# Kernel optimization log

Hardware: AMD Instinct MI355X
Metric: run time of the kernel (lower is better)

Reference implementation:

```python
import jax, jax.numpy as jnp
import numpy as np

B, N, D, K, C = 8, 4096, 128, 16, 64  # batch, points, in_channels, knn, growth_rate


def _knn_idx(pos, k):
    # pos: (B, N, 3); returns (B, N, k) nearest-neighbor indices excluding self (offset=1)
    sq = jnp.sum(pos * pos, axis=-1)  # (B, N)
    d2 = sq[:, :, None] + sq[:, None, :] - 2.0 * jnp.einsum('bnd,bmd->bnm', pos, pos)
    _, idx = jax.lax.top_k(-d2, k + 1)  # sorted ascending by distance
    return idx[:, :, 1:]


def _knn_group(x, idx):
    # x: (B, N, F), idx: (B, N, K) -> (B, N, K, F)
    return jax.vmap(lambda xb, ib: xb[ib])(x, idx)


def setup_inputs():
    key = jax.random.key(0)
    ks = jax.random.split(key, 10)
    sc = 0.05
    return {
        'x': jax.random.normal(ks[0], (B, N, D), jnp.float32),
        'pos': jax.random.normal(ks[1], (B, N, 3), jnp.float32),
        'W_first': jax.random.normal(ks[2], (3 * D, C), jnp.float32) * sc,
        'b_first': jnp.zeros((C,), jnp.float32),
        'W_mid1': jax.random.normal(ks[3], (D + C, C), jnp.float32) * sc,
        'b_mid1': jnp.zeros((C,), jnp.float32),
        'W_mid2': jax.random.normal(ks[4], (D + 2 * C, C), jnp.float32) * sc,
        'b_mid2': jnp.zeros((C,), jnp.float32),
        'W_last': jax.random.normal(ks[5], (D + 3 * C, C), jnp.float32) * sc,
        'b_last': jnp.zeros((C,), jnp.float32),
    }


def reference(x, pos, W_first, b_first, W_mid1, b_mid1, W_mid2, b_mid2, W_last, b_last):
    knn_idx = _knn_idx(pos, K)                      # (B, N, K)
    knn_feat = _knn_group(x, knn_idx)               # (B, N, K, D)
    x_tiled = jnp.broadcast_to(x[:, :, None, :], knn_feat.shape)
    edge_feat = jnp.concatenate([x_tiled, knn_feat, knn_feat - x_tiled], axis=-1)  # (B,N,K,3D)

    y = jnp.concatenate([jax.nn.relu(edge_feat @ W_first + b_first), x_tiled], axis=-1)  # (B,N,K,D+C)
    y = jnp.concatenate([jax.nn.relu(y @ W_mid1 + b_mid1), y], axis=-1)                  # (B,N,K,D+2C)
    y = jnp.concatenate([jax.nn.relu(y @ W_mid2 + b_mid2), y], axis=-1)                  # (B,N,K,D+3C)
    y = jnp.concatenate([y @ W_last + b_last, y], axis=-1)                               # (B,N,K,D+4C)
    return jnp.max(y, axis=2)                       # (B, N, D+4C)
```

## Files before the change

kernel.cpp:

```cpp
#include <hip/hip_runtime.h>
#include <hip/hip_bf16.h>

typedef unsigned int uint;
typedef unsigned short ushort_t;
typedef unsigned long long u64;
typedef __attribute__((ext_vector_type(8))) short short8;
typedef __attribute__((ext_vector_type(4))) float floatx4;

#define NB 8
#define NP 4096
#define ND 128
#define NK 16
#define NC 64
#define NPTS 32768
#define QB 16
#define CAP4 208
#define NQE 8

__device__ __forceinline__ float bf2f(ushort_t h){ return __uint_as_float(((uint)h)<<16); }
__device__ __forceinline__ ushort_t f2bf(float f){
  uint u = __float_as_uint(f);
  u = u + 0x7FFFu + ((u>>16)&1u);
  return (ushort_t)(u>>16);
}
__device__ __forceinline__ float ldin(const void* p, long i, int f32){
  return f32 ? ((const float*)p)[i] : bf2f(((const ushort_t*)p)[i]);
}
__device__ __forceinline__ void stout(void* o, long i, float v, int f32){
  if (f32) ((float*)o)[i] = v; else ((ushort_t*)o)[i] = f2bf(v);
}

#define SWZE(row, e) (((row)<<6) + ((e) ^ (((row)&7)<<3)))
#define WAVE_SYNC() asm volatile("s_waitcnt lgkmcnt(0)" ::: "memory")

__global__ __launch_bounds__(256) void k_detect(const uint* __restrict__ w, int* __restrict__ flag){
  __shared__ int cnt;
  if (threadIdx.x == 0) cnt = 0;
  __syncthreads();
  int c = 0;
  for (int i = threadIdx.x; i < 512; i += 256){
    uint u = w[i];
    uint e = (u >> 7) & 0xFFu;
    c += (e >= 100u && e < 128u) ? 1 : 0;
  }
  atomicAdd(&cnt, c);
  __syncthreads();
  if (threadIdx.x == 0) *flag = (cnt < 256) ? 1 : 0;
}

__global__ __launch_bounds__(256) void k_posf(const void* __restrict__ pos, float4* __restrict__ posf,
                                              const int* __restrict__ flag){
#pragma clang fp contract(off)
  int f32 = *flag;
  int p = blockIdx.x*256 + threadIdx.x;
  if (p >= NPTS) return;
  float x = ldin(pos, (long)p*3+0, f32);
  float y = ldin(pos, (long)p*3+1, f32);
  float z = ldin(pos, (long)p*3+2, f32);
  float px = x*x; float py = y*y; float pz = z*z;
  float sq = (px + py) + pz;
  posf[p] = make_float4(x, y, z, sq);
}

__global__ __launch_bounds__(256) void k_knn(const float4* __restrict__ posf, int* __restrict__ knn){
#pragma clang fp contract(off)
  __shared__ u64 scand[QB][CAP4];
  __shared__ int scnt[QB];
  __shared__ uint sut[QB];
  int tid = threadIdx.x;
  int lane = tid & 63;
  int wave = tid >> 6;
  int qbase = blockIdx.x * QB;
  int jbase = (qbase >> 12) << 12;
  if (tid < QB){ scnt[tid] = 0; sut[tid] = 0xFFFFFFFFu; }
  __syncthreads();
  float4 Q[QB];
  #pragma unroll
  for (int q = 0; q < QB; ++q) Q[q] = posf[qbase + q];
  float lmf[QB];
  #pragma unroll
  for (int q = 0; q < QB; ++q) lmf[q] = 3.0e38f;
  for (int s = 0; s < 16; ++s){
    float4 p = posf[jbase + s*256 + tid];
    #pragma unroll
    for (int q = 0; q < QB; ++q){
      float dot = __builtin_fmaf(Q[q].x, p.x, __builtin_fmaf(Q[q].y, p.y, Q[q].z * p.z));
      float v   = __builtin_fmaf(-2.0f, dot, Q[q].w + p.w);
      lmf[q] = fminf(lmf[q], v);
    }
  }
  uint lmb[QB];
  #pragma unroll
  for (int q = 0; q < QB; ++q) lmb[q] = __float_as_uint(fmaxf(lmf[q], 0.0f));
  #pragma unroll
  for (int q = 0; q < QB; ++q){
    int lo = 0, hi = 4095;
    while (lo < hi){
      int mid = (lo + hi) >> 1;
      uint T = (uint)(mid+1) << 19;
      u64 bal = __ballot(lmb[q] < T);
      if (__popcll(bal) >= 17) hi = mid; else lo = mid + 1;
    }
    if (lane == 0) atomicMin(&sut[q], (uint)(lo+2) << 19);
  }
  __syncthreads();
  uint utq[QB];
  #pragma unroll
  for (int q = 0; q < QB; ++q) utq[q] = sut[q];
  for (int s = 0; s < 16; ++s){
    int j = s*256 + tid;
    float4 p = posf[jbase + j];
    #pragma unroll
    for (int q = 0; q < QB; ++q){
      float ax = Q[q].x*p.x; float ay = Q[q].y*p.y; float az = Q[q].z*p.z;
      float dot = (ax + ay) + az;
      float t  = Q[q].w + p.w;
      float v  = t - 2.0f*dot;
      uint ubv = __float_as_uint(fmaxf(v, 0.0f));
      if (ubv < utq[q]){
        int pc = atomicAdd(&scnt[q], 1);
        if (pc < CAP4){
          uint w = __float_as_uint(v);
          uint sd = w ^ ((w & 0x80000000u) ? 0xFFFFFFFFu : 0x80000000u);
          scand[q][pc] = (((u64)sd) << 32) | (uint)j;
        }
      }
    }
  }
  __syncthreads();
  for (int q = wave; q < QB; q += 4){
    int cnt = scnt[q]; if (cnt > CAP4) cnt = CAP4;
    for (int base = 0; base < cnt; base += 64){
      int ci = base + lane;
      u64 mykey = (ci < cnt) ? scand[q][ci] : ~0ull;
      int r = 0;
      for (int i = 0; i < cnt; ++i) r += (scand[q][i] < mykey) ? 1 : 0;
      if (ci < cnt && r >= 1 && r <= 16)
        knn[(qbase + q)*16 + (r-1)] = (int)(mykey & 0xFFFFFFFFu);
    }
  }
}

__global__ __launch_bounds__(256) void k_wprep(const void* __restrict__ Wf, const void* __restrict__ bfv,
                        const void* __restrict__ Wm1, const void* __restrict__ bm1,
                        const void* __restrict__ Wm2, const void* __restrict__ bm2,
                        const void* __restrict__ Wl, const void* __restrict__ bl,
                        ushort_t* __restrict__ WcatT, float* __restrict__ biasT,
                        ushort_t* __restrict__ Wtiles,
                        const int* __restrict__ flag){
  int f32 = *flag;
  int id = blockIdx.x*256 + threadIdx.x;
  if (id < 40960){
    int n = id >> 7, k = id & 127;
    float v;
    if (n < 64)       v = ldin(Wf, (long)k*64 + n, f32) - ldin(Wf, (long)(256+k)*64 + n, f32);
    else if (n < 128) v = ldin(Wf, (long)(128+k)*64 + (n-64), f32) + ldin(Wf, (long)(256+k)*64 + (n-64), f32);
    else if (n < 192) v = ldin(Wm1, (long)(64+k)*64 + (n-128), f32);
    else if (n < 256) v = ldin(Wm2, (long)(128+k)*64 + (n-192), f32);
    else              v = ldin(Wl, (long)(192+k)*64 + (n-256), f32);
    WcatT[id] = f2bf(v);
  } else if (id < 41280){
    int n = id - 40960;
    float bv;
    if (n < 64)       bv = ldin(bfv, n, f32);
    else if (n < 128) bv = 0.0f;
    else if (n < 192) bv = ldin(bm1, n-128, f32);
    else if (n < 256) bv = ldin(bm2, n-192, f32);
    else              bv = ldin(bl, n-256, f32);
    biasT[n] = bv;
  } else if (id < 65856){
    int t2 = id - 41280;
    int tile = t2 >> 10;
    int r    = (t2 >> 6) & 15;
    int ep   = t2 & 63;
    int kl   = ep ^ ((r & 7) << 3);
    float v;
    if (tile < 4){
      int n = tile*16 + r;
      v = ldin(Wm1, (long)kl*64 + n, f32);
    } else if (tile < 12){
      int u = tile - 4; int n = (u >> 1)*16 + r; int k = (u & 1)*64 + kl;
      v = ldin(Wm2, (long)k*64 + n, f32);
    } else {
      int u = tile - 12; int n = (u / 3)*16 + r; int k = (u % 3)*64 + kl;
      v = ldin(Wl, (long)k*64 + n, f32);
    }
    Wtiles[t2] = f2bf(v);
  }
}

__global__ __launch_bounds__(256) void k_pgemm(const void* __restrict__ xv, const ushort_t* __restrict__ WcatT,
                                               const float* __restrict__ biasT, ushort_t* __restrict__ P,
                                               const int* __restrict__ flag){
  int f32 = *flag;
  int wave = threadIdx.x >> 6, lane = threadIdx.x & 63;
  int rowbase = blockIdx.x*64 + wave*16;
  int quad = lane >> 4, col = lane & 15;
  floatx4 acc[20];
  #pragma unroll
  for (int i = 0; i < 20; ++i) acc[i] = (floatx4){0.f,0.f,0.f,0.f};
  #pragma unroll
  for (int kk = 0; kk < 4; ++kk){
    int k = kk*32 + quad*8;
    short8 a;
    if (f32){
      const float* xf = (const float*)xv + (long)(rowbase + col)*128 + k;
      #pragma unroll
      for (int i = 0; i < 8; ++i) a[i] = (short)f2bf(xf[i]);
    } else {
      a = *(const short8*)((const ushort_t*)xv + (long)(rowbase + col)*128 + k);
    }
    #pragma unroll
    for (int nt = 0; nt < 20; ++nt){
      short8 bb = *(const short8*)(WcatT + (nt*16 + col)*128 + k);
      acc[nt] = __builtin_amdgcn_mfma_f32_16x16x32_bf16(a, bb, acc[nt], 0, 0, 0);
    }
  }
  #pragma unroll
  for (int nt = 0; nt < 20; ++nt){
    float bv = biasT[nt*16 + col];
    #pragma unroll
    for (int r = 0; r < 4; ++r){
      int m = quad*4 + r;
      P[(long)(rowbase + m)*320 + nt*16 + col] = f2bf(acc[nt][r] + bv);
    }
  }
}

__global__ __launch_bounds__(256) void k_edge(const void* __restrict__ x, const ushort_t* __restrict__ P,
                                              const int* __restrict__ knn,
                                              const ushort_t* __restrict__ Wg, void* __restrict__ out,
                                              const int* __restrict__ flag){
  __shared__ __align__(16) ushort_t wlds[24*1024];
  __shared__ __align__(16) ushort_t hb[4][3][1024];
  int f32 = *flag;
  int tid = threadIdx.x;
  int wave = tid >> 6, lane = tid & 63;
  int quad = lane >> 4, col = lane & 15;
  #pragma unroll
  for (int i = 0; i < 12; ++i){
    int e = (i*256 + tid) << 3;
    *(short8*)(wlds + e) = *(const short8*)(Wg + e);
  }
  __syncthreads();
  const ushort_t* wA = wlds;
  const ushort_t* wB = wlds + 4*1024;
  const ushort_t* wC = wlds + 12*1024;
  ushort_t* h1p = hb[wave][0];
  ushort_t* h2p = hb[wave][1];
  ushort_t* h3p = hb[wave][2];
  int qid0 = blockIdx.x*(4*NQE) + wave*NQE;

  for (int iq = 0; iq < NQE; ++iq){
    int qid = qid0 + iq;
    int b = qid >> 12;
    const ushort_t* Prow = P + (long)qid*320;
    long outb = (long)qid*384;

    float u1v[4], u2v[4], u3v[4];
    #pragma unroll
    for (int nt = 0; nt < 4; ++nt){
      u1v[nt] = bf2f(Prow[128 + nt*16 + col]);
      u2v[nt] = bf2f(Prow[192 + nt*16 + col]);
      u3v[nt] = bf2f(Prow[256 + nt*16 + col]);
    }

    {
      int e = lane >> 2, cg = lane & 3;
      int nbr = knn[qid*16 + e] & (NP - 1);
      const ushort_t* Pk = P + ((long)(b<<12) + nbr)*320 + 64 + cg*16;
      const ushort_t* Pq = Prow + cg*16;
      short8 k0 = *(const short8*)(Pk);
      short8 k1 = *(const short8*)(Pk + 8);
      short8 q0 = *(const short8*)(Pq);
      short8 q1 = *(const short8*)(Pq + 8);
      short8 h0, h1r;
      #pragma unroll
      for (int i = 0; i < 8; ++i){
        float v = fmaxf(bf2f((ushort_t)q0[i]) + bf2f((ushort_t)k0[i]), 0.0f);
        h0[i] = (short)f2bf(v);
        float w = fmaxf(bf2f((ushort_t)q1[i]) + bf2f((ushort_t)k1[i]), 0.0f);
        h1r[i] = (short)f2bf(w);
      }
      *(short8*)(h1p + SWZE(e, cg*16))     = h0;
      *(short8*)(h1p + SWZE(e, cg*16 + 8)) = h1r;
    }
    WAVE_SYNC();

    floatx4 acc2[4];
    #pragma unroll
    for (int nt = 0; nt < 4; ++nt) acc2[nt] = (floatx4){0.f,0.f,0.f,0.f};
    #pragma unroll
    for (int kk = 0; kk < 2; ++kk){
      int k = kk*32 + quad*8;
      short8 a = *(const short8*)(h1p + SWZE(col, k));
      #pragma unroll
      for (int nt = 0; nt < 4; ++nt){
        short8 bb = *(const short8*)(wA + nt*1024 + SWZE(col, k));
        acc2[nt] = __builtin_amdgcn_mfma_f32_16x16x32_bf16(a, bb, acc2[nt], 0, 0, 0);
      }
    }
    #pragma unroll
    for (int nt = 0; nt < 4; ++nt){
      float v0 = fmaxf(acc2[nt][0] + u1v[nt], 0.0f);
      float v1 = fmaxf(acc2[nt][1] + u1v[nt], 0.0f);
      float v2 = fmaxf(acc2[nt][2] + u1v[nt], 0.0f);
      float v3 = fmaxf(acc2[nt][3] + u1v[nt], 0.0f);
      h2p[SWZE(quad*4+0, nt*16+col)] = f2bf(v0);
      h2p[SWZE(quad*4+1, nt*16+col)] = f2bf(v1);
      h2p[SWZE(quad*4+2, nt*16+col)] = f2bf(v2);
      h2p[SWZE(quad*4+3, nt*16+col)] = f2bf(v3);
      float m2 = fmaxf(fmaxf(v0, v1), fmaxf(v2, v3));
      m2 = fmaxf(m2, __shfl_xor(m2, 16, 64));
      m2 = fmaxf(m2, __shfl_xor(m2, 32, 64));
      if (lane < 16) stout(out, outb + 128 + nt*16 + lane, bf2f(f2bf(m2)), f32);
    }
    WAVE_SYNC();

    floatx4 acc3[4];
    #pragma unroll
    for (int nt = 0; nt < 4; ++nt) acc3[nt] = (floatx4){0.f,0.f,0.f,0.f};
    #pragma unroll
    for (int kk = 0; kk < 4; ++kk){
      int kg = kk*32 + quad*8;
      const ushort_t* src = (kk < 2) ? h2p : h1p;
      int kl = (kk < 2) ? kg : (kg - 64);
      short8 a = *(const short8*)(src + SWZE(col, kl));
      #pragma unroll
      for (int nt = 0; nt < 4; ++nt){
        short8 bb = *(const short8*)(wB + (nt*2 + (kg>>6))*1024 + SWZE(col, kg & 63));
        acc3[nt] = __builtin_amdgcn_mfma_f32_16x16x32_bf16(a, bb, acc3[nt], 0, 0, 0);
      }
    }
    #pragma unroll
    for (int nt = 0; nt < 4; ++nt){
      float v0 = fmaxf(acc3[nt][0] + u2v[nt], 0.0f);
      float v1 = fmaxf(acc3[nt][1] + u2v[nt], 0.0f);
      float v2 = fmaxf(acc3[nt][2] + u2v[nt], 0.0f);
      float v3 = fmaxf(acc3[nt][3] + u2v[nt], 0.0f);
      h3p[SWZE(quad*4+0, nt*16+col)] = f2bf(v0);
      h3p[SWZE(quad*4+1, nt*16+col)] = f2bf(v1);
      h3p[SWZE(quad*4+2, nt*16+col)] = f2bf(v2);
      h3p[SWZE(quad*4+3, nt*16+col)] = f2bf(v3);
      float m3 = fmaxf(fmaxf(v0, v1), fmaxf(v2, v3));
      m3 = fmaxf(m3, __shfl_xor(m3, 16, 64));
      m3 = fmaxf(m3, __shfl_xor(m3, 32, 64));
      if (lane < 16) stout(out, outb + 64 + nt*16 + lane, bf2f(f2bf(m3)), f32);
    }
    WAVE_SYNC();

    floatx4 acc4[4];
    #pragma unroll
    for (int nt = 0; nt < 4; ++nt) acc4[nt] = (floatx4){0.f,0.f,0.f,0.f};
    #pragma unroll
    for (int kk = 0; kk < 6; ++kk){
      int kg = kk*32 + quad*8;
      const ushort_t* src = (kk < 2) ? h3p : ((kk < 4) ? h2p : h1p);
      int kl = (kk < 2) ? kg : ((kk < 4) ? (kg - 64) : (kg - 128));
      short8 a = *(const short8*)(src + SWZE(col, kl));
      #pragma unroll
      for (int nt = 0; nt < 4; ++nt){
        short8 bb = *(const short8*)(wC + (nt*3 + (kg>>6))*1024 + SWZE(col, kg & 63));
        acc4[nt] = __builtin_amdgcn_mfma_f32_16x16x32_bf16(a, bb, acc4[nt], 0, 0, 0);
      }
    }
    #pragma unroll
    for (int nt = 0; nt < 4; ++nt){
      float m0 = fmaxf(fmaxf(acc4[nt][0], acc4[nt][1]), fmaxf(acc4[nt][2], acc4[nt][3])) + u3v[nt];
      m0 = fmaxf(m0, __shfl_xor(m0, 16, 64));
      m0 = fmaxf(m0, __shfl_xor(m0, 32, 64));
      if (lane < 16) stout(out, outb + nt*16 + lane, m0, f32);
    }
    {
      ushort_t mx1 = 0;
      #pragma unroll
      for (int m = 0; m < 16; ++m){
        ushort_t v1u = h1p[SWZE(m, lane)]; if (v1u > mx1) mx1 = v1u;
      }
      stout(out, outb + 192 + lane, bf2f(mx1), f32);
      stout(out, outb + 256 + lane,      ldin(x, (long)qid*128 + lane, f32), f32);
      stout(out, outb + 256 + 64 + lane, ldin(x, (long)qid*128 + 64 + lane, f32), f32);
    }
    WAVE_SYNC();
  }
}

extern "C" void kernel_launch(void* const* d_in, const int* in_sizes, int n_in,
                              void* d_out, int out_size, void* d_ws, size_t ws_size,
                              hipStream_t stream){
  const void* x   = d_in[0];
  const void* pos = d_in[1];
  const void* Wf  = d_in[2];
  const void* bfv = d_in[3];
  const void* Wm1 = d_in[4];
  const void* bm1 = d_in[5];
  const void* Wm2 = d_in[6];
  const void* bm2 = d_in[7];
  const void* Wl  = d_in[8];
  const void* bl  = d_in[9];
  char* ws = (char*)d_ws;
  float4*   posf   = (float4*)(ws + 0);
  int*      knn    = (int*)(ws + 524288);
  ushort_t* P      = (ushort_t*)(ws + 2621440);
  ushort_t* WcatT  = (ushort_t*)(ws + 23592960);
  float*    biasT  = (float*)(ws + 23674880);
  ushort_t* Wtiles = (ushort_t*)(ws + 23676160);
  int*      flag   = (int*)(ws + 23725312);

  k_detect<<<1,    256, 0, stream>>>((const uint*)Wf, flag);
  k_posf <<<128,   256, 0, stream>>>(pos, posf, flag);
  k_wprep<<<258,   256, 0, stream>>>(Wf, bfv, Wm1, bm1, Wm2, bm2, Wl, bl, WcatT, biasT, Wtiles, flag);
  k_knn  <<<2048,  256, 0, stream>>>(posf, knn);
  k_pgemm<<<512,   256, 0, stream>>>(x, WcatT, biasT, P, flag);
  k_edge <<<1024,  256, 0, stream>>>(x, P, knn, Wtiles, d_out, flag);
}
```

Baseline: 358.6 us.

## Prefetch neighbor rows and interleave KNN threshold binary searches

In the KNN kernel, the lower-bound pass now folds the -2 scaling into the neighbor coordinates and adds the query's squared norm after the min. The per-query binary searches now run as a fixed 12-iteration loop over all 16 queries, so their ballots can overlap. In the MLP kernel, neighbor indices for all queries of a wave are loaded up front, and the next query's neighbor and query feature rows are prefetched into registers while the current one is processed, hiding gather latency. This raises register pressure, and the bound computation is rounded differently, though it is only used as a threshold.

New measurement: 373.9 us. 4.3% more time.

```diff
diff --git a/kernel.cpp b/kernel.cpp
--- a/kernel.cpp
+++ b/kernel.cpp
@@ -77,31 +77,40 @@
   float4 Q[QB];
   #pragma unroll
   for (int q = 0; q < QB; ++q) Q[q] = posf[qbase + q];
-  float lmf[QB];
-  #pragma unroll
-  for (int q = 0; q < QB; ++q) lmf[q] = 3.0e38f;
+  float lmg[QB];
+  #pragma unroll
+  for (int q = 0; q < QB; ++q) lmg[q] = 3.0e38f;
   for (int s = 0; s < 16; ++s){
     float4 p = posf[jbase + s*256 + tid];
+    float px2 = -2.0f*p.x, py2 = -2.0f*p.y, pz2 = -2.0f*p.z;
     #pragma unroll
     for (int q = 0; q < QB; ++q){
-      float dot = __builtin_fmaf(Q[q].x, p.x, __builtin_fmaf(Q[q].y, p.y, Q[q].z * p.z));
-      float v   = __builtin_fmaf(-2.0f, dot, Q[q].w + p.w);
-      lmf[q] = fminf(lmf[q], v);
+      float g = __builtin_fmaf(Q[q].x, px2, __builtin_fmaf(Q[q].y, py2,
+                __builtin_fmaf(Q[q].z, pz2, p.w)));
+      lmg[q] = fminf(lmg[q], g);
     }
   }
   uint lmb[QB];
   #pragma unroll
-  for (int q = 0; q < QB; ++q) lmb[q] = __float_as_uint(fmaxf(lmf[q], 0.0f));
-  #pragma unroll
-  for (int q = 0; q < QB; ++q){
-    int lo = 0, hi = 4095;
-    while (lo < hi){
-      int mid = (lo + hi) >> 1;
+  for (int q = 0; q < QB; ++q)
+    lmb[q] = __float_as_uint(fmaxf(lmg[q] + Q[q].w, 0.0f));
+  int lo[QB], hi[QB];
+  #pragma unroll
+  for (int q = 0; q < QB; ++q){ lo[q] = 0; hi[q] = 4095; }
+  for (int it = 0; it < 12; ++it){
+    #pragma unroll
+    for (int q = 0; q < QB; ++q){
+      int mid = (lo[q] + hi[q]) >> 1;
       uint T = (uint)(mid+1) << 19;
       u64 bal = __ballot(lmb[q] < T);
-      if (__popcll(bal) >= 17) hi = mid; else lo = mid + 1;
-    }
-    if (lane == 0) atomicMin(&sut[q], (uint)(lo+2) << 19);
+      bool c = __popcll(bal) >= 17;
+      hi[q] = c ? mid : hi[q];
+      lo[q] = c ? lo[q] : mid + 1;
+    }
+  }
+  #pragma unroll
+  for (int q = 0; q < QB; ++q){
+    if (lane == 0) atomicMin(&sut[q], (uint)(lo[q]+2) << 19);
   }
   __syncthreads();
   uint utq[QB];
@@ -250,10 +259,23 @@
   ushort_t* h2p = hb[wave][1];
   ushort_t* h3p = hb[wave][2];
   int qid0 = blockIdx.x*(4*NQE) + wave*NQE;
-
+  int b = qid0 >> 12;
+  const ushort_t* Pb = P + ((long)(b<<12))*320;
+  int e4 = lane >> 2, cg = lane & 3;
+
+  int idxv[NQE];
+  #pragma unroll
+  for (int iq = 0; iq < NQE; ++iq)
+    idxv[iq] = knn[(qid0+iq)*16 + e4] & (NP - 1);
+
+  short8 nk0 = *(const short8*)(Pb + (long)idxv[0]*320 + 64 + cg*16);
+  short8 nk1 = *(const short8*)(Pb + (long)idxv[0]*320 + 64 + cg*16 + 8);
+  short8 nq0 = *(const short8*)(P + (long)qid0*320 + cg*16);
+  short8 nq1 = *(const short8*)(P + (long)qid0*320 + cg*16 + 8);
+
+  #pragma unroll
   for (int iq = 0; iq < NQE; ++iq){
     int qid = qid0 + iq;
-    int b = qid >> 12;
     const ushort_t* Prow = P + (long)qid*320;
     long outb = (long)qid*384;
 
@@ -265,15 +287,15 @@
       u3v[nt] = bf2f(Prow[256 + nt*16 + col]);
     }
 
+    short8 k0 = nk0, k1 = nk1, q0 = nq0, q1 = nq1;
+    if (iq + 1 < NQE){
+      nk0 = *(const short8*)(Pb + (long)idxv[iq+1]*320 + 64 + cg*16);
+      nk1 = *(const short8*)(Pb + (long)idxv[iq+1]*320 + 64 + cg*16 + 8);
+      nq0 = *(const short8*)(P + (long)(qid+1)*320 + cg*16);
+      nq1 = *(const short8*)(P + (long)(qid+1)*320 + cg*16 + 8);
+    }
+
     {
-      int e = lane >> 2, cg = lane & 3;
-      int nbr = knn[qid*16 + e] & (NP - 1);
-      const ushort_t* Pk = P + ((long)(b<<12) + nbr)*320 + 64 + cg*16;
-      const ushort_t* Pq = Prow + cg*16;
-      short8 k0 = *(const short8*)(Pk);
-      short8 k1 = *(const short8*)(Pk + 8);
-      short8 q0 = *(const short8*)(Pq);
-      short8 q1 = *(const short8*)(Pq + 8);
       short8 h0, h1r;
       #pragma unroll
       for (int i = 0; i < 8; ++i){
@@ -282,8 +304,8 @@
         float w = fmaxf(bf2f((ushort_t)q1[i]) + bf2f((ushort_t)k1[i]), 0.0f);
         h1r[i] = (short)f2bf(w);
       }
-      *(short8*)(h1p + SWZE(e, cg*16))     = h0;
-      *(short8*)(h1p + SWZE(e, cg*16 + 8)) = h1r;
+      *(short8*)(h1p + SWZE(e4, cg*16))     = h0;
+      *(short8*)(h1p + SWZE(e4, cg*16 + 8)) = h1r;
     }
     WAVE_SYNC();
 
```
